# Kernel optimization log

Measured on AMD Instinct MI355X. Metric: run time of the kernel, lower is better.

Reference implementation:

```python
import jax, jax.numpy as jnp
import numpy as np

N_NODES = 50000
NEG_SLOPE = 0.2  # PyG GATConv default
EPS = 1e-16      # PyG softmax denominator epsilon


def gat_conv(x, W, att_src, att_dst, bias, src, dst, heads, out_ch):
    # x: [N, F_in]; W: [F_in, heads*out_ch]; att_*: [heads, out_ch]
    N = x.shape[0]
    h = (x @ W).reshape(N, heads, out_ch)              # [N,H,C]
    a_src = jnp.sum(h * att_src, axis=-1)              # [N,H]
    a_dst = jnp.sum(h * att_dst, axis=-1)              # [N,H]
    alpha = a_src[src] + a_dst[dst]                    # [E,H]
    alpha = jnp.where(alpha > 0, alpha, NEG_SLOPE * alpha)  # leaky_relu
    amax = jax.ops.segment_max(alpha, dst, num_segments=N)  # [N,H]
    amax = jnp.where(jnp.isfinite(amax), amax, 0.0)
    ex = jnp.exp(alpha - amax[dst])                    # [E,H]
    denom = jax.ops.segment_sum(ex, dst, num_segments=N)    # [N,H]
    coef = ex / (denom[dst] + EPS)                     # [E,H]
    msg = h[src] * coef[:, :, None]                    # [E,H,C]
    out = jax.ops.segment_sum(msg, dst, num_segments=N)     # [N,H,C]
    return out.reshape(N, heads * out_ch) + bias


def setup_inputs() -> dict:
    key = jax.random.key(0)
    ks = jax.random.split(key, 11)
    T, N, F = 8, N_NODES, 64
    E = 1_600_000
    x = jax.random.normal(ks[0], (T, N, F), dtype=jnp.float32)
    edge_index = jax.random.randint(ks[1], (2, E), 0, N, dtype=jnp.int64)
    s = 0.1
    return {
        "x": x,
        "edge_index": edge_index,
        "W1": jax.random.normal(ks[2], (F, 64), jnp.float32) * s,
        "att_src1": jax.random.normal(ks[3], (8, 8), jnp.float32) * s,
        "att_dst1": jax.random.normal(ks[4], (8, 8), jnp.float32) * s,
        "bias1": jax.random.normal(ks[5], (64,), jnp.float32) * s,
        "W2": jax.random.normal(ks[6], (64, F), jnp.float32) * s,
        "att_src2": jax.random.normal(ks[7], (1, F), jnp.float32) * s,
        "att_dst2": jax.random.normal(ks[8], (1, F), jnp.float32) * s,
        "bias2": jax.random.normal(ks[9], (F,), jnp.float32) * s,
    }


def reference(x, edge_index, W1, att_src1, att_dst1, bias1, W2, att_src2, att_dst2, bias2):
    N = x.shape[1]
    # PyG GATConv adds self-loops by default
    loops = jnp.arange(N, dtype=edge_index.dtype)
    src = jnp.concatenate([edge_index[0], loops])
    dst = jnp.concatenate([edge_index[1], loops])

    def step(xt):  # xt: [N, F] ; dropout is identity in eval mode
        y = jax.nn.elu(gat_conv(xt, W1, att_src1, att_dst1, bias1, src, dst, 8, 8))
        y = gat_conv(y, W2, att_src2, att_dst2, bias2, src, dst, 1, xt.shape[-1])
        return jax.nn.log_softmax(y, axis=-1)

    return jax.vmap(step)(x)  # [T, N, F]
```

## Files before the change

kernel.cpp:

```cpp
#include <hip/hip_runtime.h>
#include <hip/hip_bf16.h>
#include <math.h>


typedef __hip_bfloat16 bf16;

__device__ __forceinline__ float bf2f(unsigned short u) {
    return __uint_as_float(((unsigned int)u) << 16);
}


__global__ __launch_bounds__(256) void count_edges_kernel(const int* __restrict__ dsts,
                                                          int* cnt, int E) {
    int i = blockIdx.x * 256 + threadIdx.x;
    if (i < E) atomicAdd(&cnt[dsts[i]], 1);
}

__global__ __launch_bounds__(1024) void scan_kernel(const int* __restrict__ cnt,
                                                    int* row, int* cur, int N) {
    __shared__ int ls[1024];
    int t = threadIdx.x;
    int chunk = (N + 1023) / 1024;
    int b = t * chunk;
    int sum = 0;
    for (int i = 0; i < chunk; ++i) {
        int idx = b + i;
        if (idx < N) sum += cnt[idx] + 1;
    }
    ls[t] = sum;
    __syncthreads();
    for (int off = 1; off < 1024; off <<= 1) {
        int v = (t >= off) ? ls[t - off] : 0;
        __syncthreads();
        ls[t] += v;
        __syncthreads();
    }
    int run = (t == 0) ? 0 : ls[t - 1];
    for (int i = 0; i < chunk; ++i) {
        int idx = b + i;
        if (idx < N) {
            int c = cnt[idx] + 1;
            row[idx] = run;
            cur[idx] = run;
            run += c;
        }
    }
    if (t == 1023) row[N] = ls[1023];
}

__global__ __launch_bounds__(256) void fill_csr_kernel(const int* __restrict__ srcs,
                                                       const int* __restrict__ dsts,
                                                       int* cur, int* esrc, int E, int N) {
    int i = blockIdx.x * 256 + threadIdx.x;
    if (i >= E + N) return;
    int s, d;
    if (i < E) { s = srcs[i]; d = dsts[i]; }
    else       { s = i - E;   d = s; }
    int pos = atomicAdd(&cur[d], 1);
    esrc[pos] = s;
}


__device__ __forceinline__ float4 ld4(const float* p) { return *(const float4*)p; }
__device__ __forceinline__ float4 ld4(const bf16* p) {
    ushort4 u = *(const ushort4*)p;
    float4 r;
    r.x = bf2f(u.x); r.y = bf2f(u.y); r.z = bf2f(u.z); r.w = bf2f(u.w);
    return r;
}


template <typename TIN, int H, int C>
__global__ __launch_bounds__(256) void gemm_att_kernel(
    const TIN* __restrict__ xin,
    size_t TOFF, int XSTRIDE,
    const float* __restrict__ Wm,
    const float* __restrict__ att_s,
    const float* __restrict__ att_d,
    bf16* __restrict__ hout,
    float* __restrict__ asrc,
    float* __restrict__ adst,
    int N) {
    __shared__ float Ws[64 * 64];
    int tid = threadIdx.x;
    {
        const float4* W4 = (const float4*)Wm;
        float4* Ws4 = (float4*)Ws;
#pragma unroll
        for (int i = 0; i < 4; ++i) Ws4[tid + 256 * i] = W4[tid + 256 * i];
    }
    __syncthreads();

    int t  = blockIdx.y;
    const TIN* xt = xin + (size_t)t * TOFF;
    bf16*  ht  = hout + t * 64;
    float* ast = asrc + t * H;
    float* adt = adst + t * H;

    int c  = tid & 63;
    int wv = tid >> 6;
    int n0 = (blockIdx.x * 4 + wv) * 4;
    if (n0 >= N) return;
    int nrows = (N - n0 >= 4) ? 4 : (N - n0);

    const TIN* xb = xt + (size_t)n0 * XSTRIDE;
    float acc[4] = {0.f, 0.f, 0.f, 0.f};

#pragma unroll 2
    for (int k4 = 0; k4 < 16; ++k4) {
        float4 xv[4];
#pragma unroll
        for (int r = 0; r < 4; ++r) {
            int rr = (r < nrows) ? r : 0;
            xv[r] = ld4(xb + (size_t)rr * XSTRIDE + k4 * 4);
        }
        float w0 = Ws[(4 * k4 + 0) * 64 + c];
        float w1 = Ws[(4 * k4 + 1) * 64 + c];
        float w2 = Ws[(4 * k4 + 2) * 64 + c];
        float w3 = Ws[(4 * k4 + 3) * 64 + c];
#pragma unroll
        for (int r = 0; r < 4; ++r) {
            acc[r] = fmaf(xv[r].x, w0, acc[r]);
            acc[r] = fmaf(xv[r].y, w1, acc[r]);
            acc[r] = fmaf(xv[r].z, w2, acc[r]);
            acc[r] = fmaf(xv[r].w, w3, acc[r]);
        }
    }

    float as_w = att_s[c];
    float ad_w = att_d[c];
#pragma unroll
    for (int r = 0; r < 4; ++r) {
        if (r >= nrows) break;
        int n = n0 + r;
        float a = acc[r];
        ht[(size_t)n * 512 + c] = __float2bfloat16(a);
        float vs = a * as_w;
        float vd = a * ad_w;
#pragma unroll
        for (int off = 1; off < C; off <<= 1) {
            vs += __shfl_xor(vs, off, 64);
            vd += __shfl_xor(vd, off, 64);
        }
        if ((c % C) == 0) {
            int hd = c / C;
            ast[(size_t)n * (8 * H) + hd] = vs;
            adt[(size_t)n * (8 * H) + hd] = vd;
        }
    }
}


#define SWZ(PU, Q) __uint_as_float(__builtin_amdgcn_ds_swizzle((PU), ((Q) << 5) | 0x18))

template <int H, bool FINAL>
__global__ __launch_bounds__(256) void gat_edge_kernel(
    const bf16* __restrict__ h_all,
    const float* __restrict__ asrc_all,
    const float* __restrict__ adst_all,
    const int* __restrict__ row,
    const int* __restrict__ esrc,
    const float* __restrict__ bias,
    bf16* __restrict__ outb,
    float* __restrict__ outf,
    int N) {
    int tid  = threadIdx.x;
    int lane = tid & 63;
    int t0   = blockIdx.y * 4;
    int n    = blockIdx.x * 4 + (tid >> 6);
    if (n >= N) return;

    const char* asrcb = (const char*)asrc_all;
    const unsigned short* hb = (const unsigned short*)h_all;

    const int head = (H == 8) ? (lane >> 3) : 0;
    float adn[4];
#pragma unroll
    for (int i = 0; i < 4; ++i)
        adn[i] = adst_all[(size_t)n * (8 * H) + (t0 + i) * H + head];

    int e0  = row[n];
    int deg = row[n + 1] - e0;
    int toff = t0 * 64 + lane;

    float lsum[4] = {0.f, 0.f, 0.f, 0.f};
    float acc[4]  = {0.f, 0.f, 0.f, 0.f};

    for (int base = 0; base < deg; base += 64) {
        int cnt = deg - base; if (cnt > 64) cnt = 64;
        int sv = (lane < cnt) ? esrc[e0 + base + lane] : 0;

        if constexpr (H == 8) {
            unsigned head4 = (unsigned)(head << 2);
            unsigned l7_4  = (unsigned)((lane & 7) << 2);
#pragma unroll
            for (int sub = 0; sub < 8; ++sub) {
                if (sub * 8 >= cnt) break;
                int svj = __builtin_amdgcn_ds_bpermute(sub * 32 + l7_4, sv);
                unsigned abase = (((unsigned)svj) << 8) | head4;
                bool valid = (sub * 8 + (lane & 7) < cnt);
                float p[4];
#pragma unroll
                for (int i = 0; i < 4; ++i) {
                    float av = *(const float*)(asrcb + (abase | ((unsigned)(t0 + i) << 5)));
                    float tv = av + adn[i];
                    tv = tv > 0.f ? tv : 0.2f * tv;
                    tv = valid ? tv : -INFINITY;
                    p[i] = __expf(tv);
                    lsum[i] += p[i];
                }
                unsigned pu0 = __float_as_uint(p[0]);
                unsigned pu1 = __float_as_uint(p[1]);
                unsigned pu2 = __float_as_uint(p[2]);
                unsigned pu3 = __float_as_uint(p[3]);
#define ACC_EDGE(Q)                                                            \
    {                                                                          \
        unsigned sj = (unsigned)__builtin_amdgcn_readlane(sv, sub * 8 + (Q));  \
        const unsigned short* hrow = hb + ((size_t)sj << 9) + toff;            \
        acc[0] = fmaf(SWZ(pu0, Q), bf2f(hrow[0]),   acc[0]);                   \
        acc[1] = fmaf(SWZ(pu1, Q), bf2f(hrow[64]),  acc[1]);                   \
        acc[2] = fmaf(SWZ(pu2, Q), bf2f(hrow[128]), acc[2]);                   \
        acc[3] = fmaf(SWZ(pu3, Q), bf2f(hrow[192]), acc[3]);                   \
    }
                ACC_EDGE(0) ACC_EDGE(1) ACC_EDGE(2) ACC_EDGE(3)
                ACC_EDGE(4) ACC_EDGE(5) ACC_EDGE(6) ACC_EDGE(7)
#undef ACC_EDGE
            }
        } else {
            unsigned abase = ((unsigned)sv) << 5;
            float p[4];
#pragma unroll
            for (int i = 0; i < 4; ++i) {
                float av = *(const float*)(asrcb + (abase | ((unsigned)(t0 + i) << 2)));
                float tv = av + adn[i];
                tv = tv > 0.f ? tv : 0.2f * tv;
                tv = (lane < cnt) ? tv : -INFINITY;
                p[i] = __expf(tv);
                lsum[i] += p[i];
            }
            for (int j0 = 0; j0 < cnt; j0 += 8) {
#pragma unroll
                for (int q = 0; q < 8; ++q) {
                    int j = j0 + q;
                    unsigned sj = (unsigned)__builtin_amdgcn_readlane(sv, j);
                    const unsigned short* hrow = hb + ((size_t)sj << 9) + toff;
                    float pj0 = __uint_as_float(
                        __builtin_amdgcn_readlane(__float_as_uint(p[0]), j));
                    float pj1 = __uint_as_float(
                        __builtin_amdgcn_readlane(__float_as_uint(p[1]), j));
                    float pj2 = __uint_as_float(
                        __builtin_amdgcn_readlane(__float_as_uint(p[2]), j));
                    float pj3 = __uint_as_float(
                        __builtin_amdgcn_readlane(__float_as_uint(p[3]), j));
                    acc[0] = fmaf(pj0, bf2f(hrow[0]),   acc[0]);
                    acc[1] = fmaf(pj1, bf2f(hrow[64]),  acc[1]);
                    acc[2] = fmaf(pj2, bf2f(hrow[128]), acc[2]);
                    acc[3] = fmaf(pj3, bf2f(hrow[192]), acc[3]);
                }
            }
        }
    }

#pragma unroll
    for (int i = 0; i < 4; ++i) {
        float ls = lsum[i];
        if constexpr (H == 8) {
            ls += __shfl_xor(ls, 1, 64);
            ls += __shfl_xor(ls, 2, 64);
            ls += __shfl_xor(ls, 4, 64);
        } else {
#pragma unroll
            for (int o = 1; o < 64; o <<= 1) ls += __shfl_xor(ls, o, 64);
        }
        float v = acc[i] / (ls + 1e-16f) + bias[lane];
        if (!FINAL) {
            float y = v > 0.f ? v : expm1f(v);
            outb[(size_t)n * 512 + (t0 + i) * 64 + lane] = __float2bfloat16(y);
        } else {
            float mx = v;
#pragma unroll
            for (int off = 1; off < 64; off <<= 1) mx = fmaxf(mx, __shfl_xor(mx, off, 64));
            float ex = __expf(v - mx);
            float sm = ex;
#pragma unroll
            for (int off = 1; off < 64; off <<= 1) sm += __shfl_xor(sm, off, 64);
            outf[(size_t)(t0 + i) * N * 64 + (size_t)n * 64 + lane] =
                (v - mx) - __logf(sm);
        }
    }
}


extern "C" void kernel_launch(void* const* d_in, const int* in_sizes, int n_in,
                              void* d_out, int out_size, void* d_ws, size_t ws_size,
                              hipStream_t stream) {
    const float* x        = (const float*)d_in[0];
    const int*   eidx     = (const int*)d_in[1];
    const float* W1       = (const float*)d_in[2];
    const float* att_src1 = (const float*)d_in[3];
    const float* att_dst1 = (const float*)d_in[4];
    const float* bias1    = (const float*)d_in[5];
    const float* W2       = (const float*)d_in[6];
    const float* att_src2 = (const float*)d_in[7];
    const float* att_dst2 = (const float*)d_in[8];
    const float* bias2    = (const float*)d_in[9];
    float* dout = (float*)d_out;

    const int N = 50000;
    const int F = 64;
    const int E = in_sizes[1] / 2;
    const int T = in_sizes[0] / (N * F);
    const int NT = T * N;
    const int Etot = E + N;
    const int BPT = (N + 3) / 4;

    const int* srcs = eidx;
    const int* dsts = eidx + E;

    char* ws = (char*)d_ws;
    size_t off = 0;
    auto carve = [&](size_t bytes) -> void* {
        void* p = ws + off;
        off = (off + bytes + 255) & ~(size_t)255;
        return p;
    };
    bf16*  h_all  = (bf16*)carve((size_t)NT * 64 * sizeof(bf16));
    bf16*  y1_all = (bf16*)carve((size_t)NT * 64 * sizeof(bf16));
    float* asrc   = (float*)carve((size_t)NT * 8 * sizeof(float));
    float* adst   = (float*)carve((size_t)NT * 8 * sizeof(float));
    int*   rowp   = (int*)carve((size_t)(N + 1) * sizeof(int));
    int*   cnt    = (int*)carve((size_t)N * sizeof(int));
    int*   cur    = (int*)carve((size_t)N * sizeof(int));
    int*   esrc   = (int*)carve((size_t)Etot * sizeof(int));
    (void)ws_size;

    hipMemsetAsync(cnt, 0, (size_t)N * sizeof(int), stream);
    count_edges_kernel<<<(E + 255) / 256, 256, 0, stream>>>(dsts, cnt, E);
    scan_kernel<<<1, 1024, 0, stream>>>(cnt, rowp, cur, N);
    fill_csr_kernel<<<(E + N + 255) / 256, 256, 0, stream>>>(srcs, dsts, cur, esrc, E, N);

    dim3 ggrid((N + 15) / 16, T);
    dim3 egrid(BPT, T / 4);
    gemm_att_kernel<float, 8, 8><<<ggrid, 256, 0, stream>>>(
        x, (size_t)N * 64, 64, W1, att_src1, att_dst1, h_all, asrc, adst, N);
    gat_edge_kernel<8, false><<<egrid, 256, 0, stream>>>(
        h_all, asrc, adst, rowp, esrc, bias1, y1_all, nullptr, N);
    gemm_att_kernel<bf16, 1, 64><<<ggrid, 256, 0, stream>>>(
        y1_all, (size_t)64, 512, W2, att_src2, att_dst2, h_all, asrc, adst, N);
    gat_edge_kernel<1, true><<<egrid, 256, 0, stream>>>(
        h_all, asrc, adst, rowp, esrc, bias2, nullptr, dout, N);
}
```

Measured before the change: 1.158 ms.

## Switch node features and attention scores to timestep-major layout

Stores h, attention scores and layer-1 outputs as separate per-timestep N×64 arrays instead of interleaving all timesteps per node. The GEMM kernel becomes a flat launch over all N·T rows with contiguous stride 64. The edge kernel now gathers four separate rows per source node, one per timestep, instead of one contiguous 1KB node record. This may cost gather locality in exchange for simpler, contiguous GEMM access and output writes.

```diff
diff --git a/kernel.cpp b/kernel.cpp
--- a/kernel.cpp
+++ b/kernel.cpp
@@ -73,14 +73,13 @@
 template <typename TIN, int H, int C>
 __global__ __launch_bounds__(256) void gemm_att_kernel(
     const TIN* __restrict__ xin,
-    size_t TOFF, int XSTRIDE,
     const float* __restrict__ Wm,
     const float* __restrict__ att_s,
     const float* __restrict__ att_d,
     bf16* __restrict__ hout,
     float* __restrict__ asrc,
     float* __restrict__ adst,
-    int N) {
+    int R) {
     __shared__ float Ws[64 * 64];
     int tid = threadIdx.x;
     {
@@ -91,19 +90,13 @@
     }
     __syncthreads();
 
-    int t  = blockIdx.y;
-    const TIN* xt = xin + (size_t)t * TOFF;
-    bf16*  ht  = hout + t * 64;
-    float* ast = asrc + t * H;
-    float* adt = adst + t * H;
-
     int c  = tid & 63;
     int wv = tid >> 6;
     int n0 = (blockIdx.x * 4 + wv) * 4;
-    if (n0 >= N) return;
-    int nrows = (N - n0 >= 4) ? 4 : (N - n0);
-
-    const TIN* xb = xt + (size_t)n0 * XSTRIDE;
+    if (n0 >= R) return;
+    int nrows = (R - n0 >= 4) ? 4 : (R - n0);
+
+    const TIN* xb = xin + (size_t)n0 * 64;
     float acc[4] = {0.f, 0.f, 0.f, 0.f};
 
 #pragma unroll 2
@@ -112,7 +105,7 @@
 #pragma unroll
         for (int r = 0; r < 4; ++r) {
             int rr = (r < nrows) ? r : 0;
-            xv[r] = ld4(xb + (size_t)rr * XSTRIDE + k4 * 4);
+            xv[r] = ld4(xb + (size_t)rr * 64 + k4 * 4);
         }
         float w0 = Ws[(4 * k4 + 0) * 64 + c];
         float w1 = Ws[(4 * k4 + 1) * 64 + c];
@@ -134,7 +127,7 @@
         if (r >= nrows) break;
         int n = n0 + r;
         float a = acc[r];
-        ht[(size_t)n * 512 + c] = __float2bfloat16(a);
+        hout[(size_t)n * 64 + c] = __float2bfloat16(a);
         float vs = a * as_w;
         float vd = a * ad_w;
 #pragma unroll
@@ -144,8 +137,8 @@
         }
         if ((c % C) == 0) {
             int hd = c / C;
-            ast[(size_t)n * (8 * H) + hd] = vs;
-            adt[(size_t)n * (8 * H) + hd] = vd;
+            asrc[(size_t)n * H + hd] = vs;
+            adst[(size_t)n * H + hd] = vd;
         }
     }
 }
@@ -170,18 +163,21 @@
     int n    = blockIdx.x * 4 + (tid >> 6);
     if (n >= N) return;
 
-    const char* asrcb = (const char*)asrc_all;
-    const unsigned short* hb = (const unsigned short*)h_all;
-
     const int head = (H == 8) ? (lane >> 3) : 0;
+
+    const char* asrc_t[4];
+    const unsigned short* hb_t[4];
     float adn[4];
 #pragma unroll
-    for (int i = 0; i < 4; ++i)
-        adn[i] = adst_all[(size_t)n * (8 * H) + (t0 + i) * H + head];
+    for (int i = 0; i < 4; ++i) {
+        int tt = t0 + i;
+        asrc_t[i] = (const char*)(asrc_all + (size_t)tt * N * H);
+        hb_t[i]   = (const unsigned short*)h_all + (size_t)tt * N * 64;
+        adn[i]    = adst_all[(size_t)tt * N * H + (size_t)n * H + head];
+    }
 
     int e0  = row[n];
     int deg = row[n + 1] - e0;
-    int toff = t0 * 64 + lane;
 
     float lsum[4] = {0.f, 0.f, 0.f, 0.f};
     float acc[4]  = {0.f, 0.f, 0.f, 0.f};
@@ -197,12 +193,12 @@
             for (int sub = 0; sub < 8; ++sub) {
                 if (sub * 8 >= cnt) break;
                 int svj = __builtin_amdgcn_ds_bpermute(sub * 32 + l7_4, sv);
-                unsigned abase = (((unsigned)svj) << 8) | head4;
+                unsigned aoff = (((unsigned)svj) << 5) | head4;
                 bool valid = (sub * 8 + (lane & 7) < cnt);
                 float p[4];
 #pragma unroll
                 for (int i = 0; i < 4; ++i) {
-                    float av = *(const float*)(asrcb + (abase | ((unsigned)(t0 + i) << 5)));
+                    float av = *(const float*)(asrc_t[i] + aoff);
                     float tv = av + adn[i];
                     tv = tv > 0.f ? tv : 0.2f * tv;
                     tv = valid ? tv : -INFINITY;
@@ -216,22 +212,22 @@
 #define ACC_EDGE(Q)                                                            \
     {                                                                          \
         unsigned sj = (unsigned)__builtin_amdgcn_readlane(sv, sub * 8 + (Q));  \
-        const unsigned short* hrow = hb + ((size_t)sj << 9) + toff;            \
-        acc[0] = fmaf(SWZ(pu0, Q), bf2f(hrow[0]),   acc[0]);                   \
-        acc[1] = fmaf(SWZ(pu1, Q), bf2f(hrow[64]),  acc[1]);                   \
-        acc[2] = fmaf(SWZ(pu2, Q), bf2f(hrow[128]), acc[2]);                   \
-        acc[3] = fmaf(SWZ(pu3, Q), bf2f(hrow[192]), acc[3]);                   \
+        size_t so = (size_t)sj << 6;                      \
+        acc[0] = fmaf(SWZ(pu0, Q), bf2f((hb_t[0] + so)[lane]), acc[0]);        \
+        acc[1] = fmaf(SWZ(pu1, Q), bf2f((hb_t[1] + so)[lane]), acc[1]);        \
+        acc[2] = fmaf(SWZ(pu2, Q), bf2f((hb_t[2] + so)[lane]), acc[2]);        \
+        acc[3] = fmaf(SWZ(pu3, Q), bf2f((hb_t[3] + so)[lane]), acc[3]);        \
     }
                 ACC_EDGE(0) ACC_EDGE(1) ACC_EDGE(2) ACC_EDGE(3)
                 ACC_EDGE(4) ACC_EDGE(5) ACC_EDGE(6) ACC_EDGE(7)
 #undef ACC_EDGE
             }
         } else {
-            unsigned abase = ((unsigned)sv) << 5;
+            unsigned aoff = ((unsigned)sv) << 2;
             float p[4];
 #pragma unroll
             for (int i = 0; i < 4; ++i) {
-                float av = *(const float*)(asrcb + (abase | ((unsigned)(t0 + i) << 2)));
+                float av = *(const float*)(asrc_t[i] + aoff);
                 float tv = av + adn[i];
                 tv = tv > 0.f ? tv : 0.2f * tv;
                 tv = (lane < cnt) ? tv : -INFINITY;
@@ -243,7 +239,7 @@
                 for (int q = 0; q < 8; ++q) {
                     int j = j0 + q;
                     unsigned sj = (unsigned)__builtin_amdgcn_readlane(sv, j);
-                    const unsigned short* hrow = hb + ((size_t)sj << 9) + toff;
+                    size_t so = (size_t)sj << 6;
                     float pj0 = __uint_as_float(
                         __builtin_amdgcn_readlane(__float_as_uint(p[0]), j));
                     float pj1 = __uint_as_float(
@@ -252,10 +248,10 @@
                         __builtin_amdgcn_readlane(__float_as_uint(p[2]), j));
                     float pj3 = __uint_as_float(
                         __builtin_amdgcn_readlane(__float_as_uint(p[3]), j));
-                    acc[0] = fmaf(pj0, bf2f(hrow[0]),   acc[0]);
-                    acc[1] = fmaf(pj1, bf2f(hrow[64]),  acc[1]);
-                    acc[2] = fmaf(pj2, bf2f(hrow[128]), acc[2]);
-                    acc[3] = fmaf(pj3, bf2f(hrow[192]), acc[3]);
+                    acc[0] = fmaf(pj0, bf2f((hb_t[0] + so)[lane]), acc[0]);
+                    acc[1] = fmaf(pj1, bf2f((hb_t[1] + so)[lane]), acc[1]);
+                    acc[2] = fmaf(pj2, bf2f((hb_t[2] + so)[lane]), acc[2]);
+                    acc[3] = fmaf(pj3, bf2f((hb_t[3] + so)[lane]), acc[3]);
                 }
             }
         }
@@ -273,9 +269,10 @@
             for (int o = 1; o < 64; o <<= 1) ls += __shfl_xor(ls, o, 64);
         }
         float v = acc[i] / (ls + 1e-16f) + bias[lane];
+        size_t oidx = ((size_t)(t0 + i) * N + n) * 64 + lane;
         if (!FINAL) {
             float y = v > 0.f ? v : expm1f(v);
-            outb[(size_t)n * 512 + (t0 + i) * 64 + lane] = __float2bfloat16(y);
+            outb[oidx] = __float2bfloat16(y);
         } else {
             float mx = v;
 #pragma unroll
@@ -284,8 +281,7 @@
             float sm = ex;
 #pragma unroll
             for (int off = 1; off < 64; off <<= 1) sm += __shfl_xor(sm, off, 64);
-            outf[(size_t)(t0 + i) * N * 64 + (size_t)n * 64 + lane] =
-                (v - mx) - __logf(sm);
+            outf[oidx] = (v - mx) - __logf(sm);
         }
     }
 }
@@ -339,14 +335,14 @@
     scan_kernel<<<1, 1024, 0, stream>>>(cnt, rowp, cur, N);
     fill_csr_kernel<<<(E + N + 255) / 256, 256, 0, stream>>>(srcs, dsts, cur, esrc, E, N);
 
-    dim3 ggrid((N + 15) / 16, T);
+    int gemm_blocks = (NT + 15) / 16;
     dim3 egrid(BPT, T / 4);
-    gemm_att_kernel<float, 8, 8><<<ggrid, 256, 0, stream>>>(
-        x, (size_t)N * 64, 64, W1, att_src1, att_dst1, h_all, asrc, adst, N);
+    gemm_att_kernel<float, 8, 8><<<gemm_blocks, 256, 0, stream>>>(
+        x, W1, att_src1, att_dst1, h_all, asrc, adst, NT);
     gat_edge_kernel<8, false><<<egrid, 256, 0, stream>>>(
         h_all, asrc, adst, rowp, esrc, bias1, y1_all, nullptr, N);
-    gemm_att_kernel<bf16, 1, 64><<<ggrid, 256, 0, stream>>>(
-        y1_all, (size_t)64, 512, W2, att_src2, att_dst2, h_all, asrc, adst, N);
+    gemm_att_kernel<bf16, 1, 64><<<gemm_blocks, 256, 0, stream>>>(
+        y1_all, W2, att_src2, att_dst2, h_all, asrc, adst, NT);
     gat_edge_kernel<1, true><<<egrid, 256, 0, stream>>>(
         h_all, asrc, adst, rowp, esrc, bias2, nullptr, dout, N);
 }
```

After: 1.241 ms. 7.2% more time.
